# Kernel tuning notes

Hardware: AMD Instinct MI355X
Metric: run time of the kernel (lower is better)

## Reference

```python
import jax, jax.numpy as jnp
import numpy as np

N_NODES = 100000
N_EDGES = 1600000
IN_FEATS = 128
HEADS = 4
OUT_FEATS = 32
NEG_SLOPE = 0.2


def setup_inputs() -> dict:
    key = jax.random.key(0)
    k1, k2, k3, k4, k5, k6 = jax.random.split(key, 6)
    feat = jax.random.normal(k1, (N_NODES, IN_FEATS), dtype=jnp.float32)
    # nn.Linear(in_feats, out_feats*num_heads).weight -> [H*D_out, D_in]
    W = jax.random.normal(k2, (HEADS * OUT_FEATS, IN_FEATS), dtype=jnp.float32) * (1.0 / np.sqrt(IN_FEATS))
    attn_l = jax.random.normal(k3, (1, HEADS, OUT_FEATS), dtype=jnp.float32) * 0.1
    attn_r = jax.random.normal(k4, (1, HEADS, OUT_FEATS), dtype=jnp.float32) * 0.1
    src = jax.random.randint(k5, (N_EDGES,), 0, N_NODES, dtype=jnp.int32)
    dst = jax.random.randint(k6, (N_EDGES,), 0, N_NODES, dtype=jnp.int32)
    return {"feat": feat, "W": W, "attn_l": attn_l, "attn_r": attn_r, "src": src, "dst": dst}


def reference(feat, W, attn_l, attn_r, src, dst):
    N = feat.shape[0]
    H, D = attn_l.shape[1], attn_l.shape[2]
    # fc: feat @ W.T -> [N, H, D]
    ft = (feat @ W.T).reshape(N, H, D)
    el = jnp.sum(ft * attn_l, axis=-1)  # [N, H]
    er = jnp.sum(ft * attn_r, axis=-1)  # [N, H]
    # SDDMM edge scores (u_add_v) + leaky relu
    e = el[src] + er[dst]  # [E, H]
    e = jnp.where(e > 0, e, NEG_SLOPE * e)
    # segment softmax over edges grouped by destination node
    emax = jax.ops.segment_max(e, dst, num_segments=N)  # [N, H]
    ez = jnp.exp(e - emax[dst])
    esum = jax.ops.segment_sum(ez, dst, num_segments=N)  # [N, H]
    a = ez / esum[dst]  # [E, H]
    # weighted SpMM aggregation (u_mul_e + sum by dst)
    out = jax.ops.segment_sum(ft[src] * a[:, :, None], dst, num_segments=N)  # [N, H, D]
    return out
```

## Files before the change

### kernel.cpp

```cpp
#include <hip/hip_runtime.h>
#include <hip/hip_fp16.h>

#define IN_FEATS 128
#define HEADS 4
#define D_OUT 32
#define HD 128
#define NEG_SLOPE 0.2f

#define BSHIFT 8
#define BSIZE 256
#define CAP 4608

typedef _Float16 half8 __attribute__((ext_vector_type(8)));
typedef _Float16 half4v __attribute__((ext_vector_type(4)));
typedef float floatx4 __attribute__((ext_vector_type(4)));

#define LSTR 40

__global__ __launch_bounds__(256) void gemm_ft(const float* __restrict__ feat,
                                               const float* __restrict__ W,
                                               const float* __restrict__ al,
                                               const float* __restrict__ ar,
                                               __half* __restrict__ ft_h,
                                               float* __restrict__ el,
                                               float* __restrict__ er, int N) {
    __shared__ _Float16 Als[128 * LSTR];
    __shared__ _Float16 Wls[128 * LSTR];
    const int t = threadIdx.x;
    const int w = t >> 6, lane = t & 63, quad = lane >> 4, l15 = lane & 15;
    const int nodeBase = blockIdx.x * 128;

    floatx4 acc[2][8] = {};

    for (int kk = 0; kk < 4; ++kk) {
        const int k0 = kk * 32;
#pragma unroll
        for (int i = 0; i < 4; ++i) {
            int idx = i * 256 + t;
            int row = idx >> 3;
            int q = idx & 7;
            int node = nodeBase + row;
            float4 v = make_float4(0.f, 0.f, 0.f, 0.f);
            if (node < N) v = *(const float4*)(feat + (size_t)node * IN_FEATS + k0 + q * 4);
            half4v hv = {(_Float16)v.x, (_Float16)v.y, (_Float16)v.z, (_Float16)v.w};
            *(half4v*)&Als[row * LSTR + q * 4] = hv;
            float4 wv = *(const float4*)(W + (size_t)row * IN_FEATS + k0 + q * 4);
            half4v hw = {(_Float16)wv.x, (_Float16)wv.y, (_Float16)wv.z, (_Float16)wv.w};
            *(half4v*)&Wls[row * LSTR + q * 4] = hw;
        }
        __syncthreads();
        half8 af0 = *(half8*)&Als[(w * 32 + l15) * LSTR + quad * 8];
        half8 af1 = *(half8*)&Als[(w * 32 + 16 + l15) * LSTR + quad * 8];
        half8 bf[8];
#pragma unroll
        for (int nt = 0; nt < 8; ++nt)
            bf[nt] = *(half8*)&Wls[(nt * 16 + l15) * LSTR + quad * 8];
#pragma unroll
        for (int nt = 0; nt < 8; ++nt) {
            acc[0][nt] = __builtin_amdgcn_mfma_f32_16x16x32_f16(af0, bf[nt], acc[0][nt], 0, 0, 0);
            acc[1][nt] = __builtin_amdgcn_mfma_f32_16x16x32_f16(af1, bf[nt], acc[1][nt], 0, 0, 0);
        }
        __syncthreads();
    }

    float alv[8], arv[8];
#pragma unroll
    for (int nt = 0; nt < 8; ++nt) {
        alv[nt] = al[nt * 16 + l15];
        arv[nt] = ar[nt * 16 + l15];
    }
#pragma unroll
    for (int mt = 0; mt < 2; ++mt) {
#pragma unroll
        for (int r = 0; r < 4; ++r) {
            int node = nodeBase + w * 32 + mt * 16 + quad * 4 + r;
            bool valid = node < N;
            if (valid) {
#pragma unroll
                for (int nt = 0; nt < 8; ++nt)
                    ft_h[(size_t)node * HD + nt * 16 + l15] = __float2half(acc[mt][nt][r]);
            }
            float sl[4], sr[4];
#pragma unroll
            for (int h = 0; h < 4; ++h) {
                sl[h] = acc[mt][2 * h][r] * alv[2 * h] + acc[mt][2 * h + 1][r] * alv[2 * h + 1];
                sr[h] = acc[mt][2 * h][r] * arv[2 * h] + acc[mt][2 * h + 1][r] * arv[2 * h + 1];
#pragma unroll
                for (int off = 1; off < 16; off <<= 1) {
                    sl[h] += __shfl_xor(sl[h], off);
                    sr[h] += __shfl_xor(sr[h], off);
                }
            }
            if (valid && l15 < 4) {
                float vl = l15 == 0 ? sl[0] : l15 == 1 ? sl[1] : l15 == 2 ? sl[2] : sl[3];
                float vr = l15 == 0 ? sr[0] : l15 == 1 ? sr[1] : l15 == 2 ? sr[2] : sr[3];
                el[node * 4 + l15] = vl;
                er[node * 4 + l15] = vr;
            }
        }
    }
}

__global__ void init_cursor(int* __restrict__ bcursor, int NB) {
    int b = blockIdx.x * blockDim.x + threadIdx.x;
    if (b < NB) bcursor[b] = b * CAP;
}

__global__ __launch_bounds__(256) void bin_scatter(const int* __restrict__ src,
                                                   const int* __restrict__ dst,
                                                   int* __restrict__ bcursor,
                                                   int* __restrict__ bedge,
                                                   int E, int NB, int chunk) {
    __shared__ int cnt[512];
    __shared__ int base[512];
    int t = threadIdx.x;
    int e0 = blockIdx.x * chunk;
    if (e0 >= E) return;
    int e1 = e0 + chunk; if (e1 > E) e1 = E;
    cnt[t] = 0; cnt[t + 256] = 0;
    __syncthreads();
    for (int e = e0 + t; e < e1; e += 256)
        atomicAdd(&cnt[dst[e] >> BSHIFT], 1);
    __syncthreads();
    for (int b = t; b < NB; b += 256) {
        int c = cnt[b];
        base[b] = c ? atomicAdd(&bcursor[b], c) : 0;
    }
    __syncthreads();
    cnt[t] = 0; cnt[t + 256] = 0;
    __syncthreads();
    for (int e = e0 + t; e < e1; e += 256) {
        int d = dst[e];
        int b = d >> BSHIFT;
        int p = base[b] + atomicAdd(&cnt[b], 1);
        if (p < (b + 1) * CAP)
            bedge[p] = src[e] | ((d & (BSIZE - 1)) << 17);
    }
}

__global__ __launch_bounds__(256) void bucket_csr(const int* __restrict__ bcursor,
                                                  int* __restrict__ bedge,
                                                  int* __restrict__ row_start,
                                                  int* __restrict__ row_end, int N) {
    __shared__ int eL[CAP];
    __shared__ int cnt[256];
    __shared__ int sc[256];
    int b = blockIdx.x, t = threadIdx.x;
    int s0 = b * CAP;
    int cntE = bcursor[b] - s0;
    cnt[t] = 0;
    __syncthreads();
    for (int i = t; i < cntE; i += 256) {
        int v = bedge[s0 + i];
        eL[i] = v;
        atomicAdd(&cnt[v >> 17], 1);
    }
    __syncthreads();
    sc[t] = cnt[t];
    __syncthreads();
    for (int off = 1; off < 256; off <<= 1) {
        int v = (t >= off) ? sc[t - off] : 0;
        __syncthreads();
        sc[t] += v;
        __syncthreads();
    }
    int node0 = b << BSHIFT;
    int ex = sc[t] - cnt[t];
    if (node0 + t < N) {
        row_start[node0 + t] = s0 + ex;
        row_end[node0 + t] = s0 + sc[t];
    }
    __syncthreads();
    cnt[t] = ex;
    __syncthreads();
    for (int i = t; i < cntE; i += 256) {
        int v = eL[i];
        int p = atomicAdd(&cnt[v >> 17], 1);
        bedge[s0 + p] = v & 0x1FFFF;
    }
}

__global__ __launch_bounds__(256) void aggregate(const __half* __restrict__ ft_h,
                                                 const float* __restrict__ el,
                                                 const float* __restrict__ er,
                                                 const int* __restrict__ row_start,
                                                 const int* __restrict__ row_end,
                                                 const int* __restrict__ bedge,
                                                 float* __restrict__ out, int N) {
    int wid = threadIdx.x >> 6, lane = threadIdx.x & 63;
    int n = blockIdx.x * 4 + wid;
    if (n >= N) return;
    int start = row_start[n];
    int end = row_end[n];
    int g = lane >> 4;
    int q = lane & 15;
    int h = q >> 2;

    float er_h = er[(size_t)n * 4 + h];

    float a0 = 0.f, a1 = 0.f, a2 = 0.f, a3 = 0.f;
    float a4 = 0.f, a5 = 0.f, a6 = 0.f, a7 = 0.f;
    float ws = 0.f;
    for (int e = start + g; e < end; e += 4) {
        int s = bedge[e] & 0x1FFFF;
        float x = el[(size_t)s * 4 + h] + er_h;
        x = x > 0.f ? x : NEG_SLOPE * x;
        float w = __expf(x);
        int4 raw = *(const int4*)(ft_h + (size_t)s * HD + q * 8);
        float2 f0 = __half22float2(*(__half2*)&raw.x);
        float2 f1 = __half22float2(*(__half2*)&raw.y);
        float2 f2 = __half22float2(*(__half2*)&raw.z);
        float2 f3 = __half22float2(*(__half2*)&raw.w);
        a0 += w * f0.x; a1 += w * f0.y;
        a2 += w * f1.x; a3 += w * f1.y;
        a4 += w * f2.x; a5 += w * f2.y;
        a6 += w * f3.x; a7 += w * f3.y;
        ws += w;
    }
    a0 += __shfl_xor(a0, 16); a0 += __shfl_xor(a0, 32);
    a1 += __shfl_xor(a1, 16); a1 += __shfl_xor(a1, 32);
    a2 += __shfl_xor(a2, 16); a2 += __shfl_xor(a2, 32);
    a3 += __shfl_xor(a3, 16); a3 += __shfl_xor(a3, 32);
    a4 += __shfl_xor(a4, 16); a4 += __shfl_xor(a4, 32);
    a5 += __shfl_xor(a5, 16); a5 += __shfl_xor(a5, 32);
    a6 += __shfl_xor(a6, 16); a6 += __shfl_xor(a6, 32);
    a7 += __shfl_xor(a7, 16); a7 += __shfl_xor(a7, 32);
    ws += __shfl_xor(ws, 16); ws += __shfl_xor(ws, 32);
    float inv = ws > 0.f ? 1.0f / ws : 0.f;
    float r0 = (g == 0 ? a0 : g == 1 ? a2 : g == 2 ? a4 : a6) * inv;
    float r1 = (g == 0 ? a1 : g == 1 ? a3 : g == 2 ? a5 : a7) * inv;
    *(float2*)(out + (size_t)n * HD + q * 8 + g * 2) = make_float2(r0, r1);
}

extern "C" void kernel_launch(void* const* d_in, const int* in_sizes, int n_in,
                              void* d_out, int out_size, void* d_ws, size_t ws_size,
                              hipStream_t stream) {
    const float* feat = (const float*)d_in[0];
    const float* W    = (const float*)d_in[1];
    const float* al   = (const float*)d_in[2];
    const float* ar   = (const float*)d_in[3];
    const int* src    = (const int*)d_in[4];
    const int* dst    = (const int*)d_in[5];
    float* out        = (float*)d_out;

    const int N = in_sizes[0] / IN_FEATS;
    const int E = in_sizes[4];
    const int NB = (N + BSIZE - 1) >> BSHIFT;

    char* ws = (char*)d_ws;
    size_t off = 0;
    auto alloc = [&](size_t bytes) {
        void* p = ws + off;
        off += (bytes + 255) & ~(size_t)255;
        return p;
    };
    __half* ft_h     = (__half*)alloc((size_t)N * HD * 2);
    float* el        = (float*)alloc((size_t)N * 4 * 4);
    float* er        = (float*)alloc((size_t)N * 4 * 4);
    int*   row_start = (int*)alloc((size_t)N * 4);
    int*   row_end   = (int*)alloc((size_t)N * 4);
    int*   bcursor   = (int*)alloc(512 * 4);
    int*   bedge     = (int*)alloc((size_t)NB * CAP * 4);
    (void)ws_size;

    gemm_ft<<<(N + 127) / 128, 256, 0, stream>>>(feat, W, al, ar, ft_h, el, er, N);
    init_cursor<<<1, 512, 0, stream>>>(bcursor, NB);
    int chunk = (E + 255) / 256;
    bin_scatter<<<256, 256, 0, stream>>>(src, dst, bcursor, bedge, E, NB, chunk);
    bucket_csr<<<NB, 256, 0, stream>>>(bcursor, bedge, row_start, row_end, N);
    aggregate<<<(N + 3) / 4, 256, 0, stream>>>(ft_h, el, er, row_start, row_end, bedge, out, N);
}
```

Before: 262.2 us.

## Stage GEMM epilogue through LDS, fold cursor init, cache edges in scatter

The GEMM epilogue now writes the accumulators to shared memory and then emits ft_h as contiguous half8 vector stores. el/er are computed from those rows with plain dot products instead of shuffle reductions. The separate init_cursor launch is folded into block 0 of the GEMM kernel. bin_scatter caches the packed edge records and bucket ids in LDS so src/dst are read once, and it runs on 512 blocks instead of 256. Costs are extra LDS traffic, larger LDS use per block, and ft being rounded to fp16 before the el/er dot products.

```diff
diff --git a/kernel.cpp b/kernel.cpp
--- a/kernel.cpp
+++ b/kernel.cpp
@@ -16,6 +16,7 @@
 typedef float floatx4 __attribute__((ext_vector_type(4)));
 
 #define LSTR 40
+#define OSTR 136
 
 __global__ __launch_bounds__(256) void gemm_ft(const float* __restrict__ feat,
                                                const float* __restrict__ W,
@@ -23,12 +24,18 @@
                                                const float* __restrict__ ar,
                                                __half* __restrict__ ft_h,
                                                float* __restrict__ el,
-                                               float* __restrict__ er, int N) {
-    __shared__ _Float16 Als[128 * LSTR];
-    __shared__ _Float16 Wls[128 * LSTR];
+                                               float* __restrict__ er,
+                                               int* __restrict__ bcursor,
+                                               int N, int NB) {
+    __shared__ __align__(16) _Float16 sh[128 * OSTR];
+    _Float16* Als = sh;
+    _Float16* Wls = sh + 5120;
     const int t = threadIdx.x;
     const int w = t >> 6, lane = t & 63, quad = lane >> 4, l15 = lane & 15;
     const int nodeBase = blockIdx.x * 128;
+
+    if (blockIdx.x == 0)
+        for (int b = t; b < NB; b += 256) bcursor[b] = b * CAP;
 
     floatx4 acc[2][8] = {};
 
@@ -63,64 +70,75 @@
         __syncthreads();
     }
 
-    float alv[8], arv[8];
-#pragma unroll
-    for (int nt = 0; nt < 8; ++nt) {
-        alv[nt] = al[nt * 16 + l15];
-        arv[nt] = ar[nt * 16 + l15];
-    }
-#pragma unroll
-    for (int mt = 0; mt < 2; ++mt) {
-#pragma unroll
-        for (int r = 0; r < 4; ++r) {
-            int node = nodeBase + w * 32 + mt * 16 + quad * 4 + r;
-            bool valid = node < N;
-            if (valid) {
-#pragma unroll
-                for (int nt = 0; nt < 8; ++nt)
-                    ft_h[(size_t)node * HD + nt * 16 + l15] = __float2half(acc[mt][nt][r]);
-            }
-            float sl[4], sr[4];
-#pragma unroll
-            for (int h = 0; h < 4; ++h) {
-                sl[h] = acc[mt][2 * h][r] * alv[2 * h] + acc[mt][2 * h + 1][r] * alv[2 * h + 1];
-                sr[h] = acc[mt][2 * h][r] * arv[2 * h] + acc[mt][2 * h + 1][r] * arv[2 * h + 1];
-#pragma unroll
-                for (int off = 1; off < 16; off <<= 1) {
-                    sl[h] += __shfl_xor(sl[h], off);
-                    sr[h] += __shfl_xor(sr[h], off);
-                }
-            }
-            if (valid && l15 < 4) {
-                float vl = l15 == 0 ? sl[0] : l15 == 1 ? sl[1] : l15 == 2 ? sl[2] : sl[3];
-                float vr = l15 == 0 ? sr[0] : l15 == 1 ? sr[1] : l15 == 2 ? sr[2] : sr[3];
-                el[node * 4 + l15] = vl;
-                er[node * 4 + l15] = vr;
-            }
-        }
-    }
-}
-
-__global__ void init_cursor(int* __restrict__ bcursor, int NB) {
-    int b = blockIdx.x * blockDim.x + threadIdx.x;
-    if (b < NB) bcursor[b] = b * CAP;
-}
+#pragma unroll
+    for (int mt = 0; mt < 2; ++mt)
+#pragma unroll
+        for (int nt = 0; nt < 8; ++nt)
+#pragma unroll
+            for (int r = 0; r < 4; ++r)
+                sh[(w * 32 + mt * 16 + quad * 4 + r) * OSTR + nt * 16 + l15] =
+                    (_Float16)acc[mt][nt][r];
+    __syncthreads();
+
+    const int row = t >> 1, seg = t & 1;
+    const int node = nodeBase + row;
+    half8 hv[8];
+#pragma unroll
+    for (int j = 0; j < 8; ++j) hv[j] = *(half8*)&sh[row * OSTR + seg * 64 + j * 8];
+
+    float accl0 = 0.f, accl1 = 0.f, accr0 = 0.f, accr1 = 0.f;
+#pragma unroll
+    for (int j = 0; j < 8; ++j) {
+        float4 a0 = *(const float4*)(al + seg * 64 + j * 8);
+        float4 a1 = *(const float4*)(al + seg * 64 + j * 8 + 4);
+        float4 r0 = *(const float4*)(ar + seg * 64 + j * 8);
+        float4 r1 = *(const float4*)(ar + seg * 64 + j * 8 + 4);
+        float v0 = (float)hv[j][0], v1 = (float)hv[j][1], v2 = (float)hv[j][2], v3 = (float)hv[j][3];
+        float v4 = (float)hv[j][4], v5 = (float)hv[j][5], v6 = (float)hv[j][6], v7 = (float)hv[j][7];
+        float dl = v0 * a0.x + v1 * a0.y + v2 * a0.z + v3 * a0.w
+                 + v4 * a1.x + v5 * a1.y + v6 * a1.z + v7 * a1.w;
+        float dr = v0 * r0.x + v1 * r0.y + v2 * r0.z + v3 * r0.w
+                 + v4 * r1.x + v5 * r1.y + v6 * r1.z + v7 * r1.w;
+        if (j < 4) { accl0 += dl; accr0 += dr; }
+        else       { accl1 += dl; accr1 += dr; }
+    }
+    if (node < N) {
+#pragma unroll
+        for (int j = 0; j < 8; ++j)
+            *(half8*)(ft_h + (size_t)node * HD + seg * 64 + j * 8) = hv[j];
+        el[node * 4 + seg * 2 + 0] = accl0;
+        el[node * 4 + seg * 2 + 1] = accl1;
+        er[node * 4 + seg * 2 + 0] = accr0;
+        er[node * 4 + seg * 2 + 1] = accr1;
+    }
+}
+
+#define MAXCHUNK 3200
 
 __global__ __launch_bounds__(256) void bin_scatter(const int* __restrict__ src,
                                                    const int* __restrict__ dst,
                                                    int* __restrict__ bcursor,
                                                    int* __restrict__ bedge,
                                                    int E, int NB, int chunk) {
+    __shared__ int recL[MAXCHUNK];
+    __shared__ unsigned short bL[MAXCHUNK];
     __shared__ int cnt[512];
     __shared__ int base[512];
     int t = threadIdx.x;
     int e0 = blockIdx.x * chunk;
     if (e0 >= E) return;
     int e1 = e0 + chunk; if (e1 > E) e1 = E;
+    int ne = e1 - e0;
     cnt[t] = 0; cnt[t + 256] = 0;
     __syncthreads();
-    for (int e = e0 + t; e < e1; e += 256)
-        atomicAdd(&cnt[dst[e] >> BSHIFT], 1);
+    for (int i = t; i < ne; i += 256) {
+        int d = dst[e0 + i];
+        int s = src[e0 + i];
+        int b = d >> BSHIFT;
+        recL[i] = s | ((d & (BSIZE - 1)) << 17);
+        bL[i] = (unsigned short)b;
+        atomicAdd(&cnt[b], 1);
+    }
     __syncthreads();
     for (int b = t; b < NB; b += 256) {
         int c = cnt[b];
@@ -129,12 +147,11 @@
     __syncthreads();
     cnt[t] = 0; cnt[t + 256] = 0;
     __syncthreads();
-    for (int e = e0 + t; e < e1; e += 256) {
-        int d = dst[e];
-        int b = d >> BSHIFT;
+    for (int i = t; i < ne; i += 256) {
+        int b = bL[i];
         int p = base[b] + atomicAdd(&cnt[b], 1);
         if (p < (b + 1) * CAP)
-            bedge[p] = src[e] | ((d & (BSIZE - 1)) << 17);
+            bedge[p] = recL[i];
     }
 }
 
@@ -263,10 +280,12 @@
     int*   bedge     = (int*)alloc((size_t)NB * CAP * 4);
     (void)ws_size;
 
-    gemm_ft<<<(N + 127) / 128, 256, 0, stream>>>(feat, W, al, ar, ft_h, el, er, N);
-    init_cursor<<<1, 512, 0, stream>>>(bcursor, NB);
-    int chunk = (E + 255) / 256;
-    bin_scatter<<<256, 256, 0, stream>>>(src, dst, bcursor, bedge, E, NB, chunk);
+    gemm_ft<<<(N + 127) / 128, 256, 0, stream>>>(feat, W, al, ar, ft_h, el, er, bcursor, N, NB);
+    int grid2 = 512;
+    int chunk = (E + grid2 - 1) / grid2;
+    if (chunk > MAXCHUNK) chunk = MAXCHUNK;
+    int nblk = (E + chunk - 1) / chunk;
+    bin_scatter<<<nblk, 256, 0, stream>>>(src, dst, bcursor, bedge, E, NB, chunk);
     bucket_csr<<<NB, 256, 0, stream>>>(bcursor, bedge, row_start, row_end, N);
     aggregate<<<(N + 3) / 4, 256, 0, stream>>>(ft_h, el, er, row_start, row_end, bedge, out, N);
 }
```

New measurement: 257.3 us. No clear change (-1.9%).
